# Kernel tuning notes

Measured on AMD Instinct MI355X. Metric: run time of the kernel, lower is better.

The kernel has to match this reference:

```python
import jax, jax.numpy as jnp
import numpy as np

N_NODES = 100000
N_EDGES = 3200000
IN_Z = 32
PROJ_H = 64
LOOP_D = 32
DEC_H = 64


def setup_inputs() -> dict:
    key = jax.random.key(0)
    ks = jax.random.split(key, 10)
    z_mod = jax.random.normal(ks[0], (N_NODES, IN_Z), dtype=jnp.float32)
    edge_index = jax.random.randint(ks[1], (2, N_EDGES), 0, N_NODES, dtype=jnp.int64)
    # loop_proj: Linear(32->64), ReLU, Linear(64->32)
    w1 = jax.random.normal(ks[2], (IN_Z, PROJ_H), dtype=jnp.float32) / np.sqrt(IN_Z)
    b1 = jnp.zeros((PROJ_H,), dtype=jnp.float32)
    w2 = jax.random.normal(ks[3], (PROJ_H, LOOP_D), dtype=jnp.float32) / np.sqrt(PROJ_H)
    b2 = jnp.zeros((LOOP_D,), dtype=jnp.float32)
    # decoder: Linear(2*loop_dim -> dec_hidden), ReLU, Linear(dec_hidden -> 1)
    dw1 = jax.random.normal(ks[4], (2 * LOOP_D, DEC_H), dtype=jnp.float32) / np.sqrt(2 * LOOP_D)
    db1 = jnp.zeros((DEC_H,), dtype=jnp.float32)
    dw2 = jax.random.normal(ks[5], (DEC_H, 1), dtype=jnp.float32) / np.sqrt(DEC_H)
    db2 = jnp.zeros((1,), dtype=jnp.float32)
    return {"z_mod": z_mod, "edge_index": edge_index, "w1": w1, "b1": b1,
            "w2": w2, "b2": b2, "dw1": dw1, "db1": db1, "dw2": dw2, "db2": db2}


def reference(z_mod, edge_index, w1, b1, w2, b2, dw1, db1, dw2, db2):
    # loop_proj: z_mod -> z_loop  [N, loop_dim]
    h = jax.nn.relu(z_mod @ w1 + b1)
    z_loop = h @ w2 + b2
    # edge-wise decoder: gather, concat, MLP
    zi = z_loop[edge_index[0]]            # [E, loop_dim]
    zj = z_loop[edge_index[1]]            # [E, loop_dim]
    he = jnp.concatenate([zi, zj], axis=-1)  # [E, 2*loop_dim]
    he = jax.nn.relu(he @ dw1 + db1)         # [E, dec_hidden]
    logits = (he @ dw2 + db2)[..., 0]        # [E]
    return logits
```

## Files before the change

### kernel.cpp

```cpp
#include <hip/hip_runtime.h>


typedef short bfrag4 __attribute__((ext_vector_type(4)));
typedef float f32x4v __attribute__((ext_vector_type(4)));
typedef int   i32x4  __attribute__((ext_vector_type(4)));

#define N_NODES 100000
#define N_EDGES 3200000

__device__ __forceinline__ unsigned short f2bf(float f) {
    unsigned int i = __float_as_uint(f);
    unsigned int r = i + 0x7FFFu + ((i >> 16) & 1u);
    return (unsigned short)(r >> 16);
}

__device__ __forceinline__ float bf2f(unsigned short b) {
    unsigned int u = ((unsigned int)b) << 16;
    return __uint_as_float(u);
}

__device__ __forceinline__ bfrag4 cvt4(float x0, float x1, float x2, float x3) {
    bfrag4 v;
    v[0] = (short)f2bf(x0);
    v[1] = (short)f2bf(x1);
    v[2] = (short)f2bf(x2);
    v[3] = (short)f2bf(x3);
    return v;
}

__global__ __launch_bounds__(256) void node_proj_kernel(
    const float* __restrict__ z_mod,
    const float* __restrict__ w1,
    const float* __restrict__ b1,
    const float* __restrict__ w2,
    const float* __restrict__ b2,
    char*           __restrict__ z8,
    unsigned short* __restrict__ scg)
{
    __shared__ unsigned short hbuf[4][16 * 72];

    const int tid  = threadIdx.x;
    const int wave = tid >> 6;
    const int lane = tid & 63;
    const int quad = lane >> 4;
    const int col  = lane & 15;

    bfrag4 bw1[2][4];
    float  bias1[4];
    for (int t = 0; t < 4; ++t) {
        const int n = col + 16 * t;
        for (int s = 0; s < 2; ++s)
            for (int j = 0; j < 4; ++j)
                bw1[s][t][j] = (short)f2bf(w1[(s * 16 + quad * 4 + j) * 64 + n]);
        bias1[t] = b1[n];
    }
    bfrag4 bw2[4][2];
    float  bias2[2];
    for (int t = 0; t < 2; ++t) {
        const int n = col + 16 * t;
        for (int s = 0; s < 4; ++s)
            for (int j = 0; j < 4; ++j)
                bw2[s][t][j] = (short)f2bf(w2[(s * 16 + quad * 4 + j) * 32 + n]);
        bias2[t] = b2[n];
    }

    unsigned short* hrow = &hbuf[wave][0];

    const int gwave  = blockIdx.x * 4 + wave;
    const int nwaves = gridDim.x * 4;
    const int ntiles = N_NODES / 16;

    for (int tile = gwave; tile < ntiles; tile += nwaves) {
        const int node0 = tile * 16;
        const float* zrow = z_mod + (size_t)(node0 + col) * 32;

        f32x4v za0 = *(const f32x4v*)(zrow + 0 * 16 + quad * 4);
        f32x4v za1 = *(const f32x4v*)(zrow + 1 * 16 + quad * 4);
        bfrag4 a10 = cvt4(za0[0], za0[1], za0[2], za0[3]);
        bfrag4 a11 = cvt4(za1[0], za1[1], za1[2], za1[3]);

        f32x4v acc[4];
        for (int t = 0; t < 4; ++t) {
            f32x4v c = {bias1[t], bias1[t], bias1[t], bias1[t]};
            c = __builtin_amdgcn_mfma_f32_16x16x16bf16_1k(a10, bw1[0][t], c, 0, 0, 0);
            c = __builtin_amdgcn_mfma_f32_16x16x16bf16_1k(a11, bw1[1][t], c, 0, 0, 0);
            acc[t] = c;
        }

        for (int t = 0; t < 4; ++t)
            for (int r = 0; r < 4; ++r) {
                float v = acc[t][r];
                v = v > 0.f ? v : 0.f;
                hrow[(quad * 4 + r) * 72 + (col + 16 * t)] = f2bf(v);
            }
        asm volatile("" ::: "memory");

        f32x4v acc2[2];
        for (int t = 0; t < 2; ++t)
            acc2[t] = (f32x4v){bias2[t], bias2[t], bias2[t], bias2[t]};
        for (int s = 0; s < 4; ++s) {
            bfrag4 a2 = *(const bfrag4*)(hrow + col * 72 + s * 16 + quad * 4);
            for (int t = 0; t < 2; ++t)
                acc2[t] = __builtin_amdgcn_mfma_f32_16x16x16bf16_1k(a2, bw2[s][t], acc2[t], 0, 0, 0);
        }
        asm volatile("" ::: "memory");

        float am[4];
        for (int r = 0; r < 4; ++r)
            am[r] = fmaxf(fabsf(acc2[0][r]), fabsf(acc2[1][r]));
        for (int mask = 1; mask <= 8; mask <<= 1)
            for (int r = 0; r < 4; ++r)
                am[r] = fmaxf(am[r], __shfl_xor(am[r], mask, 64));
        const float gm = fmaxf(fmaxf(am[0], am[1]), fmaxf(am[2], am[3]));
        const float inv = 127.f / fmaxf(gm, 1e-30f);

        char* hb = (char*)hrow;
        for (int r = 0; r < 4; ++r)
            for (int t = 0; t < 2; ++t) {
                int q = (int)rintf(acc2[t][r] * inv);
                hb[(quad * 4 + r) * 32 + (col + 16 * t)] = (char)q;
            }
        if (col == 0)
            scg[(node0 >> 2) + quad] = f2bf(gm * (1.f / 127.f));
        asm volatile("" ::: "memory");

        *(unsigned long long*)(z8 + (size_t)node0 * 32 + lane * 8) =
            *(const unsigned long long*)(hb + lane * 8);
        asm volatile("" ::: "memory");
    }
}

__global__ __launch_bounds__(256) void edge_dec_kernel(
    const int*            __restrict__ eidx,
    const char*           __restrict__ z8,
    const unsigned short* __restrict__ scg,
    const float*          __restrict__ dw1,
    const float*          __restrict__ db1,
    const float*          __restrict__ dw2,
    const float*          __restrict__ db2,
    float* __restrict__ out)
{
    const int tid  = threadIdx.x;
    const int lane = tid & 63;
    const int quad = lane >> 4;
    const int col  = lane & 15;
    const int ss   = quad >> 1;
    const int hf   = quad & 1;

    i32x4  awq[4];
    float  wscv[4];
    for (int mt = 0; mt < 4; ++mt) {
        const int m = 16 * mt + col;
        float w[16];
        float mx = 0.f;
        for (int j = 0; j < 16; ++j) {
            w[j] = dw1[(quad * 16 + j) * 64 + m];
            mx = fmaxf(mx, fabsf(w[j]));
        }
        mx = fmaxf(mx, __shfl_xor(mx, 16, 64));
        mx = fmaxf(mx, __shfl_xor(mx, 32, 64));
        wscv[mt] = mx * (1.f / 127.f);
        const float winv = 127.f / fmaxf(mx, 1e-30f);
        i32x4 a;
        for (int rr = 0; rr < 4; ++rr) {
            int pk = 0;
            for (int bi = 0; bi < 4; ++bi) {
                int q = (int)rintf(w[rr * 4 + bi] * winv);
                pk |= (q & 0xFF) << (8 * bi);
            }
            a[rr] = pk;
        }
        awq[mt] = a;
    }
    float wsce[4][4], bias1v[4][4], w2v[4][4];
    for (int mt = 0; mt < 4; ++mt)
        for (int r = 0; r < 4; ++r) {
            wsce[mt][r]   = __shfl(wscv[mt], quad * 4 + r, 64);
            bias1v[mt][r] = db1[16 * mt + quad * 4 + r];
            w2v[mt][r]    = dw2[16 * mt + quad * 4 + r];
        }
    const float bias2 = db2[0];
    const int mlo = (quad < 2) ? -1 : 0;
    const int mhi = ~mlo;

    const int gwave  = blockIdx.x * 4 + (tid >> 6);
    const int nwaves = gridDim.x * 4;
    const int npairs = N_EDGES / 32;

    const int iofs = ss * N_EDGES + col;

    int iA = eidx[gwave * 32 + iofs];
    int iB = eidx[gwave * 32 + 16 + iofs];

    for (int p = gwave; p < npairs; p += nwaves) {
        const int e0 = p * 32;

        i32x4 gA = *(const i32x4*)(z8 + (size_t)iA * 32 + hf * 16);
        i32x4 gB = *(const i32x4*)(z8 + (size_t)iB * 32 + hf * 16);
        float scA = bf2f(scg[iA >> 2]);
        float scB = bf2f(scg[iB >> 2]);

        const int pn = p + nwaves;
        const int pc = pn < npairs ? pn : gwave;
        iA = eidx[pc * 32 + iofs];
        iB = eidx[pc * 32 + 16 + iofs];

        const i32x4 zc = {0, 0, 0, 0};

        i32x4 b1, b2;
        for (int i = 0; i < 4; ++i) { b1[i] = gA[i] & mlo; b2[i] = gA[i] & mhi; }
        i32x4 a1[4], a2[4];
        for (int mt = 0; mt < 4; ++mt) {
            a1[mt] = __builtin_amdgcn_mfma_i32_16x16x64_i8(awq[mt], b1, zc, 0, 0, 0);
            a2[mt] = __builtin_amdgcn_mfma_i32_16x16x64_i8(awq[mt], b2, zc, 0, 0, 0);
        }
        float si = __shfl(scA, col, 64);
        float sj = __shfl(scA, 32 + col, 64);
        float pA = 0.f;
        for (int mt = 0; mt < 4; ++mt)
            for (int r = 0; r < 4; ++r) {
                float t = (float)a1[mt][r] * si;
                t = fmaf((float)a2[mt][r], sj, t);
                float h = fmaf(t, wsce[mt][r], bias1v[mt][r]);
                h = h > 0.f ? h : 0.f;
                pA = fmaf(h, w2v[mt][r], pA);
            }
        pA += __shfl_xor(pA, 16, 64);
        pA += __shfl_xor(pA, 32, 64);

        for (int i = 0; i < 4; ++i) { b1[i] = gB[i] & mlo; b2[i] = gB[i] & mhi; }
        for (int mt = 0; mt < 4; ++mt) {
            a1[mt] = __builtin_amdgcn_mfma_i32_16x16x64_i8(awq[mt], b1, zc, 0, 0, 0);
            a2[mt] = __builtin_amdgcn_mfma_i32_16x16x64_i8(awq[mt], b2, zc, 0, 0, 0);
        }
        si = __shfl(scB, col, 64);
        sj = __shfl(scB, 32 + col, 64);
        float pB = 0.f;
        for (int mt = 0; mt < 4; ++mt)
            for (int r = 0; r < 4; ++r) {
                float t = (float)a1[mt][r] * si;
                t = fmaf((float)a2[mt][r], sj, t);
                float h = fmaf(t, wsce[mt][r], bias1v[mt][r]);
                h = h > 0.f ? h : 0.f;
                pB = fmaf(h, w2v[mt][r], pB);
            }
        pB += __shfl_xor(pB, 16, 64);
        pB += __shfl_xor(pB, 32, 64);

        if (lane < 32) {
            float v = (lane < 16 ? pA : pB) + bias2;
            out[e0 + lane] = v;
        }
    }
}

extern "C" void kernel_launch(void* const* d_in, const int* in_sizes, int n_in,
                              void* d_out, int out_size, void* d_ws, size_t ws_size,
                              hipStream_t stream) {
    const float* z_mod = (const float*)d_in[0];
    const int*   eidx  = (const int*)d_in[1];
    const float* w1    = (const float*)d_in[2];
    const float* b1    = (const float*)d_in[3];
    const float* w2    = (const float*)d_in[4];
    const float* b2    = (const float*)d_in[5];
    const float* dw1   = (const float*)d_in[6];
    const float* db1   = (const float*)d_in[7];
    const float* dw2   = (const float*)d_in[8];
    const float* db2   = (const float*)d_in[9];
    float* out = (float*)d_out;

    char*           z8  = (char*)d_ws;
    unsigned short* scg = (unsigned short*)((char*)d_ws + (size_t)N_NODES * 32);

    node_proj_kernel<<<512, 256, 0, stream>>>(z_mod, w1, b1, w2, b2, z8, scg);
    edge_dec_kernel<<<2048, 256, 0, stream>>>(eidx, z8, scg, dw1, db1, dw2, db2, out);
}
```

Measured before the change: 167.2 us.

## Use a single global int8 scale for node embeddings to fuse edge MFMAs

Node projections are first written as bf16 into the output buffer, a global absolute maximum is found with an atomic, and a new kernel quantizes everything to int8 with that single scale. With one shared scale, the edge decoder no longer needs per-node scale gathers or the masked split into separate i and j halves. The full 64-wide concat goes through one int8 MFMA per tile, and the scales are folded into the bias and output weights. This halves the MFMA count and drops the scale lookups, but adds a memset, an extra kernel and a bf16 round trip, and a global scale may lose precision compared with per-group scales.

```diff
diff --git a/kernel.cpp b/kernel.cpp
--- a/kernel.cpp
+++ b/kernel.cpp
@@ -34,8 +34,8 @@
     const float* __restrict__ b1,
     const float* __restrict__ w2,
     const float* __restrict__ b2,
-    char*           __restrict__ z8,
-    unsigned short* __restrict__ scg)
+    unsigned short* __restrict__ z16,
+    unsigned int*   __restrict__ gmax)
 {
     __shared__ unsigned short hbuf[4][16 * 72];
 
@@ -70,6 +70,8 @@
     const int nwaves = gridDim.x * 4;
     const int ntiles = N_NODES / 16;
 
+    float wmax = 0.f;
+
     for (int tile = gwave; tile < ntiles; tile += nwaves) {
         const int node0 = tile * 16;
         const float* zrow = z_mod + (size_t)(node0 + col) * 32;
@@ -105,39 +107,52 @@
         }
         asm volatile("" ::: "memory");
 
-        float am[4];
-        for (int r = 0; r < 4; ++r)
-            am[r] = fmaxf(fabsf(acc2[0][r]), fabsf(acc2[1][r]));
-        for (int mask = 1; mask <= 8; mask <<= 1)
-            for (int r = 0; r < 4; ++r)
-                am[r] = fmaxf(am[r], __shfl_xor(am[r], mask, 64));
-        const float gm = fmaxf(fmaxf(am[0], am[1]), fmaxf(am[2], am[3]));
-        const float inv = 127.f / fmaxf(gm, 1e-30f);
-
-        char* hb = (char*)hrow;
-        for (int r = 0; r < 4; ++r)
-            for (int t = 0; t < 2; ++t) {
-                int q = (int)rintf(acc2[t][r] * inv);
-                hb[(quad * 4 + r) * 32 + (col + 16 * t)] = (char)q;
-            }
-        if (col == 0)
-            scg[(node0 >> 2) + quad] = f2bf(gm * (1.f / 127.f));
-        asm volatile("" ::: "memory");
-
-        *(unsigned long long*)(z8 + (size_t)node0 * 32 + lane * 8) =
-            *(const unsigned long long*)(hb + lane * 8);
-        asm volatile("" ::: "memory");
-    }
+        for (int t = 0; t < 2; ++t)
+            for (int r = 0; r < 4; ++r) {
+                float v = acc2[t][r];
+                wmax = fmaxf(wmax, fabsf(v));
+                z16[(size_t)(node0 + quad * 4 + r) * 32 + (col + 16 * t)] =
+                    f2bf(v);
+            }
+    }
+
+    for (int mask = 1; mask <= 32; mask <<= 1)
+        wmax = fmaxf(wmax, __shfl_xor(wmax, mask, 64));
+    if (lane == 0)
+        atomicMax(gmax, __float_as_uint(wmax));
+}
+
+__global__ __launch_bounds__(256) void quant8_kernel(
+    const unsigned short* __restrict__ z16,
+    const unsigned int*   __restrict__ gmax,
+    char* __restrict__ z8)
+{
+    const int idx = blockIdx.x * 256 + threadIdx.x;
+    if (idx >= N_NODES * 32 / 8) return;
+    const float M   = __uint_as_float(*gmax);
+    const float inv = 127.f / fmaxf(M, 1e-30f);
+
+    i32x4 v = *(const i32x4*)(z16 + (size_t)idx * 8);
+    unsigned long long pk = 0;
+#pragma unroll
+    for (int i = 0; i < 4; ++i) {
+        unsigned int w = (unsigned int)v[i];
+        int q0 = (int)rintf(bf2f((unsigned short)(w & 0xFFFF)) * inv);
+        int q1 = (int)rintf(bf2f((unsigned short)(w >> 16)) * inv);
+        pk |= ((unsigned long long)(q0 & 0xFF)) << (16 * i);
+        pk |= ((unsigned long long)(q1 & 0xFF)) << (16 * i + 8);
+    }
+    *(unsigned long long*)(z8 + (size_t)idx * 8) = pk;
 }
 
 __global__ __launch_bounds__(256) void edge_dec_kernel(
-    const int*            __restrict__ eidx,
-    const char*           __restrict__ z8,
-    const unsigned short* __restrict__ scg,
-    const float*          __restrict__ dw1,
-    const float*          __restrict__ db1,
-    const float*          __restrict__ dw2,
-    const float*          __restrict__ db2,
+    const int*          __restrict__ eidx,
+    const char*         __restrict__ z8,
+    const unsigned int* __restrict__ gmax,
+    const float*        __restrict__ dw1,
+    const float*        __restrict__ db1,
+    const float*        __restrict__ dw2,
+    const float*        __restrict__ db2,
     float* __restrict__ out)
 {
     const int tid  = threadIdx.x;
@@ -147,8 +162,10 @@
     const int ss   = quad >> 1;
     const int hf   = quad & 1;
 
-    i32x4  awq[4];
-    float  wscv[4];
+    const float gz = __uint_as_float(*gmax) * (1.f / 127.f);
+
+    i32x4 awq[4];
+    float wscv[4];
     for (int mt = 0; mt < 4; ++mt) {
         const int m = 16 * mt + col;
         float w[16];
@@ -172,16 +189,14 @@
         }
         awq[mt] = a;
     }
-    float wsce[4][4], bias1v[4][4], w2v[4][4];
+    float bS[4][4], wS[4][4];
     for (int mt = 0; mt < 4; ++mt)
         for (int r = 0; r < 4; ++r) {
-            wsce[mt][r]   = __shfl(wscv[mt], quad * 4 + r, 64);
-            bias1v[mt][r] = db1[16 * mt + quad * 4 + r];
-            w2v[mt][r]    = dw2[16 * mt + quad * 4 + r];
+            const float S = __shfl(wscv[mt], quad * 4 + r, 64) * gz;
+            bS[mt][r] = db1[16 * mt + quad * 4 + r] / S;
+            wS[mt][r] = dw2[16 * mt + quad * 4 + r] * S;
         }
     const float bias2 = db2[0];
-    const int mlo = (quad < 2) ? -1 : 0;
-    const int mhi = ~mlo;
 
     const int gwave  = blockIdx.x * 4 + (tid >> 6);
     const int nwaves = gridDim.x * 4;
@@ -197,8 +212,6 @@
 
         i32x4 gA = *(const i32x4*)(z8 + (size_t)iA * 32 + hf * 16);
         i32x4 gB = *(const i32x4*)(z8 + (size_t)iB * 32 + hf * 16);
-        float scA = bf2f(scg[iA >> 2]);
-        float scB = bf2f(scg[iB >> 2]);
 
         const int pn = p + nwaves;
         const int pc = pn < npairs ? pn : gwave;
@@ -206,44 +219,24 @@
         iB = eidx[pc * 32 + 16 + iofs];
 
         const i32x4 zc = {0, 0, 0, 0};
-
-        i32x4 b1, b2;
-        for (int i = 0; i < 4; ++i) { b1[i] = gA[i] & mlo; b2[i] = gA[i] & mhi; }
-        i32x4 a1[4], a2[4];
+        i32x4 aA[4], aB[4];
         for (int mt = 0; mt < 4; ++mt) {
-            a1[mt] = __builtin_amdgcn_mfma_i32_16x16x64_i8(awq[mt], b1, zc, 0, 0, 0);
-            a2[mt] = __builtin_amdgcn_mfma_i32_16x16x64_i8(awq[mt], b2, zc, 0, 0, 0);
-        }
-        float si = __shfl(scA, col, 64);
-        float sj = __shfl(scA, 32 + col, 64);
-        float pA = 0.f;
+            aA[mt] = __builtin_amdgcn_mfma_i32_16x16x64_i8(awq[mt], gA, zc, 0, 0, 0);
+            aB[mt] = __builtin_amdgcn_mfma_i32_16x16x64_i8(awq[mt], gB, zc, 0, 0, 0);
+        }
+
+        float pA = 0.f, pB = 0.f;
         for (int mt = 0; mt < 4; ++mt)
             for (int r = 0; r < 4; ++r) {
-                float t = (float)a1[mt][r] * si;
-                t = fmaf((float)a2[mt][r], sj, t);
-                float h = fmaf(t, wsce[mt][r], bias1v[mt][r]);
-                h = h > 0.f ? h : 0.f;
-                pA = fmaf(h, w2v[mt][r], pA);
+                float hA = (float)aA[mt][r] + bS[mt][r];
+                float hB = (float)aB[mt][r] + bS[mt][r];
+                hA = hA > 0.f ? hA : 0.f;
+                hB = hB > 0.f ? hB : 0.f;
+                pA = fmaf(hA, wS[mt][r], pA);
+                pB = fmaf(hB, wS[mt][r], pB);
             }
         pA += __shfl_xor(pA, 16, 64);
         pA += __shfl_xor(pA, 32, 64);
-
-        for (int i = 0; i < 4; ++i) { b1[i] = gB[i] & mlo; b2[i] = gB[i] & mhi; }
-        for (int mt = 0; mt < 4; ++mt) {
-            a1[mt] = __builtin_amdgcn_mfma_i32_16x16x64_i8(awq[mt], b1, zc, 0, 0, 0);
-            a2[mt] = __builtin_amdgcn_mfma_i32_16x16x64_i8(awq[mt], b2, zc, 0, 0, 0);
-        }
-        si = __shfl(scB, col, 64);
-        sj = __shfl(scB, 32 + col, 64);
-        float pB = 0.f;
-        for (int mt = 0; mt < 4; ++mt)
-            for (int r = 0; r < 4; ++r) {
-                float t = (float)a1[mt][r] * si;
-                t = fmaf((float)a2[mt][r], sj, t);
-                float h = fmaf(t, wsce[mt][r], bias1v[mt][r]);
-                h = h > 0.f ? h : 0.f;
-                pB = fmaf(h, w2v[mt][r], pB);
-            }
         pB += __shfl_xor(pB, 16, 64);
         pB += __shfl_xor(pB, 32, 64);
 
@@ -269,9 +262,12 @@
     const float* db2   = (const float*)d_in[9];
     float* out = (float*)d_out;
 
-    char*           z8  = (char*)d_ws;
-    unsigned short* scg = (unsigned short*)((char*)d_ws + (size_t)N_NODES * 32);
-
-    node_proj_kernel<<<512, 256, 0, stream>>>(z_mod, w1, b1, w2, b2, z8, scg);
-    edge_dec_kernel<<<2048, 256, 0, stream>>>(eidx, z8, scg, dw1, db1, dw2, db2, out);
-}
+    char*         z8   = (char*)d_ws;
+    unsigned int* gmax = (unsigned int*)((char*)d_ws + (size_t)N_NODES * 32);
+    unsigned short* z16 = (unsigned short*)d_out;
+
+    hipMemsetAsync(gmax, 0, 4, stream);
+    node_proj_kernel<<<512, 256, 0, stream>>>(z_mod, w1, b1, w2, b2, z16, gmax);
+    quant8_kernel<<<1563, 256, 0, stream>>>(z16, gmax, z8);
+    edge_dec_kernel<<<2048, 256, 0, stream>>>(eidx, z8, gmax, dw1, db1, dw2, db2, out);
+}
```

After: 171.9 us. 2.8% more time.
